# Kernel optimization log

Hardware: AMD Instinct MI355X
Metric: run time of the kernel (lower is better)

## Reference

```python
import jax, jax.numpy as jnp
import numpy as np

B = 8192          # number of nodes / batch
DEG = 32          # neighbors per node (fixed-degree instance of the ragged pattern)
E = B * DEG       # total neighbor rows
D = 256           # embedding_dim
A = 128           # attn_dim
ACT = 512         # action_dim
SLOPE = 0.2       # leakyrelu slope


def setup_inputs() -> dict:
    key = jax.random.key(0)
    ks = jax.random.split(key, 12)
    inp = {
        "state": jax.random.normal(ks[0], (B, 2 * D), jnp.float32),
        "now_embedding": jax.random.normal(ks[1], (B, D), jnp.float32),
        "neigh": jax.random.normal(ks[2], (E, D), jnp.float32),
        "seg_ids": jnp.repeat(jnp.arange(B, dtype=jnp.int32), DEG),  # sorted segment ids
        # attention projection Linear(D, A)
        "attn_w": jax.random.normal(ks[3], (D, A), jnp.float32) * (1.0 / np.sqrt(D)),
        "attn_b": jnp.zeros((A,), jnp.float32),
        # attn_weight Linear(2A, 1)
        "aw_w": jax.random.normal(ks[4], (2 * A, 1), jnp.float32) * (1.0 / np.sqrt(2 * A)),
        "aw_b": jnp.zeros((1,), jnp.float32),
        # MLP head
        "w1": jax.random.normal(ks[5], (3 * D, 512), jnp.float32) * (1.0 / np.sqrt(3 * D)),
        "b1": jnp.zeros((512,), jnp.float32),
        "w2": jax.random.normal(ks[6], (512, 1024), jnp.float32) * (1.0 / np.sqrt(512)),
        "b2": jnp.zeros((1024,), jnp.float32),
        "w3": jax.random.normal(ks[7], (1024, ACT), jnp.float32) * (1.0 / np.sqrt(1024)),
        "b3": jnp.zeros((ACT,), jnp.float32),
    }
    return inp


def reference(state, now_embedding, neigh, seg_ids, attn_w, attn_b, aw_w, aw_b,
              w1, b1, w2, b2, w3, b3):
    # project center and neighbor embeddings to attn space
    now_proj = now_embedding @ attn_w + attn_b          # [B, A]
    nb_proj = neigh @ attn_w + attn_b                   # [E, A]
    # attn_weight applied to concat([now_proj[seg], nb_proj]) == split matvec
    w_now, w_nb = aw_w[:A, 0], aw_w[A:, 0]              # [A], [A]
    scores = (now_proj @ w_now)[seg_ids] + nb_proj @ w_nb + aw_b[0]   # [E]
    scores = jnp.where(scores >= 0, scores, SLOPE * scores)           # LeakyReLU(0.2)
    # per-segment (per-node) softmax over neighbors
    seg_max = jax.ops.segment_max(scores, seg_ids, num_segments=B)
    e = jnp.exp(scores - seg_max[seg_ids])
    seg_sum = jax.ops.segment_sum(e, seg_ids, num_segments=B)
    alpha = e / seg_sum[seg_ids]                        # [E]
    # weighted aggregation of raw neighbor embeddings
    agg = jax.ops.segment_sum(alpha[:, None] * neigh, seg_ids, num_segments=B)  # [B, D]
    # MLP head (dropout prob = 0 -> identity)
    out = jnp.concatenate([state, agg], axis=1)         # [B, 3D]
    out = jax.nn.relu(out @ w1 + b1)
    out = jax.nn.relu(out @ w2 + b2)
    out = out @ w3 + b3
    return jax.nn.softmax(out, axis=-1)
```

## Files before the change

### kernel.cpp

```cpp
#include <hip/hip_runtime.h>
#include <hip/hip_bf16.h>

#define B_SEG  8192
#define DEG    32
#define D_DIM  256
#define TWO_D  512
#define H1     512
#define H2     1024
#define ACTD   512
#define SLOPE  0.2f

typedef __attribute__((ext_vector_type(8))) short bf16x8;
typedef __attribute__((ext_vector_type(4))) float f32x4;

#define OFF_VNOW  ((size_t)0)
#define OFF_VNB   ((size_t)1024)
#define OFF_CNST  ((size_t)2048)
#define OFF_W1T   ((size_t)4096)
#define OFF_W2T   (OFF_W1T + (size_t)768*512*2)
#define OFF_W3T   (OFF_W2T + (size_t)512*1024*2)
#define OFF_X1    (OFF_W3T + (size_t)1024*512*2)
#define OFF_X2    (OFF_X1 + (size_t)B_SEG*768*2)
#define OFF_X3    (OFF_X2 + (size_t)B_SEG*512*2)
#define OFF_LOG   (OFF_X3 + (size_t)B_SEG*1024*2)

typedef const unsigned int __attribute__((address_space(1)))* gas_ptr;
typedef unsigned int __attribute__((address_space(3)))* las_ptr;

__device__ __forceinline__ void gload_lds16(const void* g, void* l) {
    __builtin_amdgcn_global_load_lds((gas_ptr)g, (las_ptr)l, 16, 0, 0);
}

__global__ __launch_bounds__(256) void prep_all(
        const float* __restrict__ attn_w, const float* __restrict__ attn_b,
        const float* __restrict__ aw_w, const float* __restrict__ aw_b,
        const float* __restrict__ w1, const float* __restrict__ w2, const float* __restrict__ w3,
        float* __restrict__ vnow, float* __restrict__ vnb, float* __restrict__ cnst,
        __hip_bfloat16* __restrict__ w1T, __hip_bfloat16* __restrict__ w2T,
        __hip_bfloat16* __restrict__ w3T) {
    int bid = blockIdx.x;
    if (bid == 0) {
        const int d = threadIdx.x;
        float s0 = 0.f, s1 = 0.f;
        for (int a = 0; a < 128; ++a) {
            const float w = attn_w[d * 128 + a];
            s0 = fmaf(w, aw_w[a], s0);
            s1 = fmaf(w, aw_w[128 + a], s1);
        }
        vnow[d] = s0;
        vnb[d]  = s1;
        if (d == 0) {
            float c = aw_b[0];
            for (int a = 0; a < 128; ++a) c = fmaf(attn_b[a], aw_w[a] + aw_w[128 + a], c);
            cnst[0] = c;
        }
        return;
    }
    bid -= 1;
    const float* src;
    __hip_bfloat16* dst;
    int K, N;
    if (bid < 384)      { src = w1; dst = w1T; K = 768;  N = 512;  }
    else if (bid < 896) { bid -= 384; src = w2; dst = w2T; K = 512;  N = 1024; }
    else                { bid -= 896; src = w3; dst = w3T; K = 1024; N = 512;  }
    const int tk = K >> 5;
    const int bk = (bid % tk) * 32;
    const int bn = (bid / tk) * 32;

    __shared__ float tile[32][33];
    const int tx = threadIdx.x & 31;
    const int ty = threadIdx.x >> 5;
#pragma unroll
    for (int i = 0; i < 32; i += 8)
        tile[ty + i][tx] = src[(size_t)(bk + ty + i) * N + (bn + tx)];
    __syncthreads();
#pragma unroll
    for (int i = 0; i < 32; i += 8)
        dst[(size_t)(bn + ty + i) * K + (bk + tx)] = __float2bfloat16(tile[tx][ty + i]);
}

__global__ __launch_bounds__(256) void attn_fused(
        const float* __restrict__ state, const float* __restrict__ now_emb,
        const float* __restrict__ neigh, const float* __restrict__ vnow,
        const float* __restrict__ vnb, const float* __restrict__ cnst,
        __hip_bfloat16* __restrict__ X1) {
    const int b    = blockIdx.x;
    const int tid  = threadIdx.x;
    const int lane = tid & 63;
    const int w    = tid >> 6;
    const int l4   = lane * 4;

    __shared__ float s_score[DEG];
    __shared__ float s_now;
    __shared__ float s_part[4][D_DIM];

    const float4 vb = *(const float4*)&vnb[l4];
    float4 nv[8];
#pragma unroll
    for (int i = 0; i < 8; ++i) {
        const int e = w * 8 + i;
        nv[i] = *(const float4*)&neigh[((size_t)b * DEG + e) * D_DIM + l4];
        float p = nv[i].x * vb.x + nv[i].y * vb.y + nv[i].z * vb.z + nv[i].w * vb.w;
#pragma unroll
        for (int off = 32; off; off >>= 1) p += __shfl_xor(p, off);
        if (lane == 0) s_score[e] = p;
    }
    if (w == 0) {
        const float4 va = *(const float4*)&vnow[l4];
        const float4 ne = *(const float4*)&now_emb[(size_t)b * D_DIM + l4];
        float p = ne.x * va.x + ne.y * va.y + ne.z * va.z + ne.w * va.w;
#pragma unroll
        for (int off = 32; off; off >>= 1) p += __shfl_xor(p, off);
        if (lane == 0) s_now = p + cnst[0];
    }
    __syncthreads();

    if (w == 0) {
        float s = (lane < DEG) ? (s_score[lane] + s_now) : -3.4e38f;
        s = (s >= 0.f) ? s : SLOPE * s;
        float m = s;
#pragma unroll
        for (int off = 32; off; off >>= 1) m = fmaxf(m, __shfl_xor(m, off));
        const float e = (lane < DEG) ? expf(s - m) : 0.f;
        float t = e;
#pragma unroll
        for (int off = 32; off; off >>= 1) t += __shfl_xor(t, off);
        if (lane < DEG) s_score[lane] = e / t;
    }
    __syncthreads();

    float4 part = {0.f, 0.f, 0.f, 0.f};
#pragma unroll
    for (int i = 0; i < 8; ++i) {
        const float al = s_score[w * 8 + i];
        part.x = fmaf(al, nv[i].x, part.x);
        part.y = fmaf(al, nv[i].y, part.y);
        part.z = fmaf(al, nv[i].z, part.z);
        part.w = fmaf(al, nv[i].w, part.w);
    }
    *(float4*)&s_part[w][l4] = part;
    __syncthreads();

    const float a = s_part[0][tid] + s_part[1][tid] + s_part[2][tid] + s_part[3][tid];

    __hip_bfloat16* xrow = X1 + (size_t)b * 768;
    xrow[512 + tid] = __float2bfloat16(a);
    const float2 st = *(const float2*)&state[(size_t)b * TWO_D + 2 * tid];
    __hip_bfloat162 h;
    h.x = __float2bfloat16(st.x);
    h.y = __float2bfloat16(st.y);
    *(__hip_bfloat162*)&xrow[2 * tid] = h;
}

template <int RELU, int OUTF32>
__global__ __launch_bounds__(256) void gemm_mfma(
        const __hip_bfloat16* __restrict__ A, const __hip_bfloat16* __restrict__ BT,
        const float* __restrict__ bias, void* __restrict__ Cout, int N, int K) {
    __shared__ __hip_bfloat16 sA[64 * 32];
    __shared__ __hip_bfloat16 sB[128 * 32];

    const int tid  = threadIdx.x;
    const int lane = tid & 63;
    const int wv   = tid >> 6;
    const int wr   = wv >> 1;
    const int wc   = wv & 1;
    const size_t mBase = (size_t)blockIdx.x * 64;
    const size_t nBase = (size_t)blockIdx.y * 128;

    f32x4 acc[2][4];
#pragma unroll
    for (int r = 0; r < 2; ++r)
#pragma unroll
        for (int c = 0; c < 4; ++c) acc[r][c] = (f32x4){0.f, 0.f, 0.f, 0.f};

    const int srow = tid >> 2;
    const int sseg = tid & 3;
    const __hip_bfloat16* gA  = A  + (mBase + srow) * (size_t)K + sseg * 8;
    const __hip_bfloat16* gB0 = BT + (nBase + srow) * (size_t)K + sseg * 8;
    const __hip_bfloat16* gB1 = gB0 + (size_t)64 * K;
    char* ldsA = (char*)&sA[0] + tid * 16;
    char* ldsB = (char*)&sB[0] + tid * 16;

    const int fr  = lane & 15;
    const int fkb = (lane >> 4) * 16;

    for (int k0 = 0; k0 < K; k0 += 32) {
        gload_lds16(gA + k0, ldsA);
        gload_lds16(gB0 + k0, ldsB);
        gload_lds16(gB1 + k0, ldsB + 4096);
        __syncthreads();

        bf16x8 aF[2], bF[4];
#pragma unroll
        for (int r = 0; r < 2; ++r)
            aF[r] = *(const bf16x8*)((const char*)sA + (wr * 32 + r * 16 + fr) * 64 + fkb);
#pragma unroll
        for (int c = 0; c < 4; ++c)
            bF[c] = *(const bf16x8*)((const char*)sB + (wc * 64 + c * 16 + fr) * 64 + fkb);
#pragma unroll
        for (int r = 0; r < 2; ++r)
#pragma unroll
            for (int c = 0; c < 4; ++c)
                acc[r][c] = __builtin_amdgcn_mfma_f32_16x16x32_bf16(aF[r], bF[c], acc[r][c], 0, 0, 0);
        __syncthreads();
    }

    const int fq = lane >> 4;
#pragma unroll
    for (int r = 0; r < 2; ++r) {
#pragma unroll
        for (int c = 0; c < 4; ++c) {
            const size_t col = nBase + wc * 64 + c * 16 + fr;
            const float bcol = bias[col];
#pragma unroll
            for (int q = 0; q < 4; ++q) {
                const size_t row = mBase + wr * 32 + r * 16 + fq * 4 + q;
                float v = acc[r][c][q] + bcol;
                if (RELU) v = fmaxf(v, 0.f);
                if (OUTF32) ((float*)Cout)[row * N + col] = v;
                else ((__hip_bfloat16*)Cout)[row * N + col] = __float2bfloat16(v);
            }
        }
    }
}

__global__ __launch_bounds__(256) void softmax512(const float* __restrict__ logits,
                                                  float* __restrict__ out) {
    const int b    = blockIdx.x;
    const int tid  = threadIdx.x;
    const int lane = tid & 63;
    const int w    = tid >> 6;
    const float* row = logits + (size_t)b * ACTD;
    const float x0 = row[tid], x1 = row[tid + 256];
    float m = fmaxf(x0, x1);
#pragma unroll
    for (int off = 32; off; off >>= 1) m = fmaxf(m, __shfl_xor(m, off));
    __shared__ float sm[4], ss[4];
    if (lane == 0) sm[w] = m;
    __syncthreads();
    m = fmaxf(fmaxf(sm[0], sm[1]), fmaxf(sm[2], sm[3]));
    const float e0 = expf(x0 - m), e1 = expf(x1 - m);
    float t = e0 + e1;
#pragma unroll
    for (int off = 32; off; off >>= 1) t += __shfl_xor(t, off);
    if (lane == 0) ss[w] = t;
    __syncthreads();
    const float inv = 1.f / (ss[0] + ss[1] + ss[2] + ss[3]);
    out[(size_t)b * ACTD + tid]       = e0 * inv;
    out[(size_t)b * ACTD + tid + 256] = e1 * inv;
}

extern "C" void kernel_launch(void* const* d_in, const int* in_sizes, int n_in,
                              void* d_out, int out_size, void* d_ws, size_t ws_size,
                              hipStream_t stream) {
    const float* state   = (const float*)d_in[0];
    const float* now_emb = (const float*)d_in[1];
    const float* neigh   = (const float*)d_in[2];
    const float* attn_w  = (const float*)d_in[4];
    const float* attn_b  = (const float*)d_in[5];
    const float* aw_w    = (const float*)d_in[6];
    const float* aw_b    = (const float*)d_in[7];
    const float* w1      = (const float*)d_in[8];
    const float* b1      = (const float*)d_in[9];
    const float* w2      = (const float*)d_in[10];
    const float* b2      = (const float*)d_in[11];
    const float* w3      = (const float*)d_in[12];
    const float* b3      = (const float*)d_in[13];
    float* out = (float*)d_out;

    char* ws = (char*)d_ws;
    float*          vnow = (float*)(ws + OFF_VNOW);
    float*          vnb  = (float*)(ws + OFF_VNB);
    float*          cnst = (float*)(ws + OFF_CNST);
    __hip_bfloat16* w1T  = (__hip_bfloat16*)(ws + OFF_W1T);
    __hip_bfloat16* w2T  = (__hip_bfloat16*)(ws + OFF_W2T);
    __hip_bfloat16* w3T  = (__hip_bfloat16*)(ws + OFF_W3T);
    __hip_bfloat16* X1   = (__hip_bfloat16*)(ws + OFF_X1);
    __hip_bfloat16* X2   = (__hip_bfloat16*)(ws + OFF_X2);
    __hip_bfloat16* X3   = (__hip_bfloat16*)(ws + OFF_X3);
    float*          lgts = (float*)(ws + OFF_LOG);

    prep_all<<<1409, 256, 0, stream>>>(attn_w, attn_b, aw_w, aw_b, w1, w2, w3,
                                       vnow, vnb, cnst, w1T, w2T, w3T);
    attn_fused<<<B_SEG, 256, 0, stream>>>(state, now_emb, neigh, vnow, vnb, cnst, X1);
    gemm_mfma<1, 0><<<dim3(128, 4), 256, 0, stream>>>(X1, w1T, b1, (void*)X2, 512, 768);
    gemm_mfma<1, 0><<<dim3(128, 8), 256, 0, stream>>>(X2, w2T, b2, (void*)X3, 1024, 512);
    gemm_mfma<0, 1><<<dim3(128, 4), 256, 0, stream>>>(X3, w3T, b3, (void*)lgts, 512, 1024);
    softmax512<<<B_SEG, 256, 0, stream>>>(lgts, out);
}
```

Before: 141.7 us.

## Fuse final GEMM with row softmax and fold weight transposes into attention kernel

The last GEMM now has each 512-thread block compute a full 32x512 row slab and apply bias plus a row softmax in registers, using cross-wave reductions through LDS. This removes the fp32 logits round trip through global memory and the separate softmax launch. The weight transpose/bf16 cast blocks are appended to the attention kernel's grid so they run alongside attention work, leaving only a tiny one-block prep launch before it. In exchange, every GEMM3 block streams the whole w3T, so weight traffic rises, and with 256 blocks and no double buffering the fused GEMM may have less latency hiding.

```diff
diff --git a/kernel.cpp b/kernel.cpp
--- a/kernel.cpp
+++ b/kernel.cpp
@@ -5,8 +5,6 @@
 #define DEG    32
 #define D_DIM  256
 #define TWO_D  512
-#define H1     512
-#define H2     1024
 #define ACTD   512
 #define SLOPE  0.2f
 
@@ -22,7 +20,6 @@
 #define OFF_X1    (OFF_W3T + (size_t)1024*512*2)
 #define OFF_X2    (OFF_X1 + (size_t)B_SEG*768*2)
 #define OFF_X3    (OFF_X2 + (size_t)B_SEG*512*2)
-#define OFF_LOG   (OFF_X3 + (size_t)B_SEG*1024*2)
 
 typedef const unsigned int __attribute__((address_space(1)))* gas_ptr;
 typedef unsigned int __attribute__((address_space(3)))* las_ptr;
@@ -31,68 +28,71 @@
     __builtin_amdgcn_global_load_lds((gas_ptr)g, (las_ptr)l, 16, 0, 0);
 }
 
-__global__ __launch_bounds__(256) void prep_all(
+__global__ __launch_bounds__(256) void prep_vec(
         const float* __restrict__ attn_w, const float* __restrict__ attn_b,
         const float* __restrict__ aw_w, const float* __restrict__ aw_b,
-        const float* __restrict__ w1, const float* __restrict__ w2, const float* __restrict__ w3,
-        float* __restrict__ vnow, float* __restrict__ vnb, float* __restrict__ cnst,
-        __hip_bfloat16* __restrict__ w1T, __hip_bfloat16* __restrict__ w2T,
-        __hip_bfloat16* __restrict__ w3T) {
-    int bid = blockIdx.x;
-    if (bid == 0) {
-        const int d = threadIdx.x;
-        float s0 = 0.f, s1 = 0.f;
-        for (int a = 0; a < 128; ++a) {
-            const float w = attn_w[d * 128 + a];
-            s0 = fmaf(w, aw_w[a], s0);
-            s1 = fmaf(w, aw_w[128 + a], s1);
-        }
-        vnow[d] = s0;
-        vnb[d]  = s1;
-        if (d == 0) {
-            float c = aw_b[0];
-            for (int a = 0; a < 128; ++a) c = fmaf(attn_b[a], aw_w[a] + aw_w[128 + a], c);
-            cnst[0] = c;
-        }
-        return;
-    }
-    bid -= 1;
-    const float* src;
-    __hip_bfloat16* dst;
-    int K, N;
-    if (bid < 384)      { src = w1; dst = w1T; K = 768;  N = 512;  }
-    else if (bid < 896) { bid -= 384; src = w2; dst = w2T; K = 512;  N = 1024; }
-    else                { bid -= 896; src = w3; dst = w3T; K = 1024; N = 512;  }
-    const int tk = K >> 5;
-    const int bk = (bid % tk) * 32;
-    const int bn = (bid / tk) * 32;
-
-    __shared__ float tile[32][33];
-    const int tx = threadIdx.x & 31;
-    const int ty = threadIdx.x >> 5;
-#pragma unroll
-    for (int i = 0; i < 32; i += 8)
-        tile[ty + i][tx] = src[(size_t)(bk + ty + i) * N + (bn + tx)];
-    __syncthreads();
-#pragma unroll
-    for (int i = 0; i < 32; i += 8)
-        dst[(size_t)(bn + ty + i) * K + (bk + tx)] = __float2bfloat16(tile[tx][ty + i]);
-}
-
-__global__ __launch_bounds__(256) void attn_fused(
+        float* __restrict__ vnow, float* __restrict__ vnb, float* __restrict__ cnst) {
+    const int d = threadIdx.x;
+    float s0 = 0.f, s1 = 0.f;
+    for (int a = 0; a < 128; ++a) {
+        const float w = attn_w[d * 128 + a];
+        s0 = fmaf(w, aw_w[a], s0);
+        s1 = fmaf(w, aw_w[128 + a], s1);
+    }
+    vnow[d] = s0;
+    vnb[d]  = s1;
+    if (d == 0) {
+        float c = aw_b[0];
+        for (int a = 0; a < 128; ++a) c = fmaf(attn_b[a], aw_w[a] + aw_w[128 + a], c);
+        cnst[0] = c;
+    }
+}
+
+__global__ __launch_bounds__(256) void attn_tr(
         const float* __restrict__ state, const float* __restrict__ now_emb,
         const float* __restrict__ neigh, const float* __restrict__ vnow,
         const float* __restrict__ vnb, const float* __restrict__ cnst,
-        __hip_bfloat16* __restrict__ X1) {
-    const int b    = blockIdx.x;
+        __hip_bfloat16* __restrict__ X1,
+        const float* __restrict__ w1, const float* __restrict__ w2,
+        const float* __restrict__ w3,
+        __hip_bfloat16* __restrict__ w1T, __hip_bfloat16* __restrict__ w2T,
+        __hip_bfloat16* __restrict__ w3T) {
+    __shared__ __align__(16) float smem[1088];
+    const int bid = blockIdx.x;
+
+    if (bid >= B_SEG) {
+        int pb = bid - B_SEG;
+        const float* src;
+        __hip_bfloat16* dst;
+        int K, N;
+        if (pb < 384)      { src = w1; dst = w1T; K = 768;  N = 512;  }
+        else if (pb < 896) { pb -= 384; src = w2; dst = w2T; K = 512;  N = 1024; }
+        else               { pb -= 896; src = w3; dst = w3T; K = 1024; N = 512;  }
+        const int tk = K >> 5;
+        const int bk = (pb % tk) * 32;
+        const int bn = (pb / tk) * 32;
+        float (*tile)[33] = (float(*)[33])smem;
+        const int tx = threadIdx.x & 31;
+        const int ty = threadIdx.x >> 5;
+#pragma unroll
+        for (int i = 0; i < 32; i += 8)
+            tile[ty + i][tx] = src[(size_t)(bk + ty + i) * N + (bn + tx)];
+        __syncthreads();
+#pragma unroll
+        for (int i = 0; i < 32; i += 8)
+            dst[(size_t)(bn + ty + i) * K + (bk + tx)] = __float2bfloat16(tile[tx][ty + i]);
+        return;
+    }
+
+    const int b    = bid;
     const int tid  = threadIdx.x;
     const int lane = tid & 63;
     const int w    = tid >> 6;
     const int l4   = lane * 4;
 
-    __shared__ float s_score[DEG];
-    __shared__ float s_now;
-    __shared__ float s_part[4][D_DIM];
+    float* s_part  = smem;
+    float* s_score = smem + 1024;
+    float* s_now   = smem + 1056;
 
     const float4 vb = *(const float4*)&vnb[l4];
     float4 nv[8];
@@ -111,12 +111,12 @@
         float p = ne.x * va.x + ne.y * va.y + ne.z * va.z + ne.w * va.w;
 #pragma unroll
         for (int off = 32; off; off >>= 1) p += __shfl_xor(p, off);
-        if (lane == 0) s_now = p + cnst[0];
+        if (lane == 0) s_now[0] = p + cnst[0];
     }
     __syncthreads();
 
     if (w == 0) {
-        float s = (lane < DEG) ? (s_score[lane] + s_now) : -3.4e38f;
+        float s = (lane < DEG) ? (s_score[lane] + s_now[0]) : -3.4e38f;
         s = (s >= 0.f) ? s : SLOPE * s;
         float m = s;
 #pragma unroll
@@ -138,10 +138,11 @@
         part.z = fmaf(al, nv[i].z, part.z);
         part.w = fmaf(al, nv[i].w, part.w);
     }
-    *(float4*)&s_part[w][l4] = part;
-    __syncthreads();
-
-    const float a = s_part[0][tid] + s_part[1][tid] + s_part[2][tid] + s_part[3][tid];
+    *(float4*)&s_part[w * D_DIM + l4] = part;
+    __syncthreads();
+
+    const float a = s_part[tid] + s_part[D_DIM + tid] + s_part[2 * D_DIM + tid] +
+                    s_part[3 * D_DIM + tid];
 
     __hip_bfloat16* xrow = X1 + (size_t)b * 768;
     xrow[512 + tid] = __float2bfloat16(a);
@@ -224,30 +225,140 @@
     }
 }
 
-__global__ __launch_bounds__(256) void softmax512(const float* __restrict__ logits,
-                                                  float* __restrict__ out) {
-    const int b    = blockIdx.x;
+__global__ __launch_bounds__(512) void gemm3_softmax(
+        const __hip_bfloat16* __restrict__ A, const __hip_bfloat16* __restrict__ BT,
+        const float* __restrict__ bias, float* __restrict__ out) {
+    constexpr int K = 1024;
+    constexpr int N = 512;
+    __shared__ __hip_bfloat16 sA[32 * 32];
+    __shared__ __hip_bfloat16 sB[512 * 32];
+    __shared__ float s_max[8][32];
+    __shared__ float s_sum[8][32];
+    __shared__ float s_gmax[32];
+    __shared__ float s_ginv[32];
+
     const int tid  = threadIdx.x;
     const int lane = tid & 63;
-    const int w    = tid >> 6;
-    const float* row = logits + (size_t)b * ACTD;
-    const float x0 = row[tid], x1 = row[tid + 256];
-    float m = fmaxf(x0, x1);
-#pragma unroll
-    for (int off = 32; off; off >>= 1) m = fmaxf(m, __shfl_xor(m, off));
-    __shared__ float sm[4], ss[4];
-    if (lane == 0) sm[w] = m;
-    __syncthreads();
-    m = fmaxf(fmaxf(sm[0], sm[1]), fmaxf(sm[2], sm[3]));
-    const float e0 = expf(x0 - m), e1 = expf(x1 - m);
-    float t = e0 + e1;
-#pragma unroll
-    for (int off = 32; off; off >>= 1) t += __shfl_xor(t, off);
-    if (lane == 0) ss[w] = t;
-    __syncthreads();
-    const float inv = 1.f / (ss[0] + ss[1] + ss[2] + ss[3]);
-    out[(size_t)b * ACTD + tid]       = e0 * inv;
-    out[(size_t)b * ACTD + tid + 256] = e1 * inv;
+    const int wv   = tid >> 6;
+    const size_t mBase = (size_t)blockIdx.x * 32;
+
+    f32x4 acc[2][4];
+#pragma unroll
+    for (int r = 0; r < 2; ++r)
+#pragma unroll
+        for (int c = 0; c < 4; ++c) acc[r][c] = (f32x4){0.f, 0.f, 0.f, 0.f};
+
+    const __hip_bfloat16* gA = A + (mBase + (tid >> 2)) * (size_t)K + (tid & 3) * 8;
+    char* ldsA = (char*)&sA[0] + tid * 16;
+    const __hip_bfloat16* gB[4];
+    char* ldsB[4];
+#pragma unroll
+    for (int i = 0; i < 4; ++i) {
+        const int s = tid + i * 512;
+        gB[i]   = BT + (size_t)(s >> 2) * K + (s & 3) * 8;
+        ldsB[i] = (char*)&sB[0] + s * 16;
+    }
+
+    const int fr  = lane & 15;
+    const int fkb = (lane >> 4) * 16;
+
+    for (int k0 = 0; k0 < K; k0 += 32) {
+        if (tid < 128) gload_lds16(gA + k0, ldsA);
+#pragma unroll
+        for (int i = 0; i < 4; ++i) gload_lds16(gB[i] + k0, ldsB[i]);
+        __syncthreads();
+
+        bf16x8 aF[2], bF[4];
+#pragma unroll
+        for (int r = 0; r < 2; ++r)
+            aF[r] = *(const bf16x8*)((const char*)sA + (r * 16 + fr) * 64 + fkb);
+#pragma unroll
+        for (int c = 0; c < 4; ++c)
+            bF[c] = *(const bf16x8*)((const char*)sB + (wv * 64 + c * 16 + fr) * 64 + fkb);
+#pragma unroll
+        for (int r = 0; r < 2; ++r)
+#pragma unroll
+            for (int c = 0; c < 4; ++c)
+                acc[r][c] = __builtin_amdgcn_mfma_f32_16x16x32_bf16(aF[r], bF[c], acc[r][c], 0, 0, 0);
+        __syncthreads();
+    }
+
+    const int fq = lane >> 4;
+    float bcol[4];
+#pragma unroll
+    for (int c = 0; c < 4; ++c) bcol[c] = bias[wv * 64 + c * 16 + fr];
+
+    float rm[2][4];
+#pragma unroll
+    for (int r = 0; r < 2; ++r)
+#pragma unroll
+        for (int q = 0; q < 4; ++q) {
+            float m = -3.4e38f;
+#pragma unroll
+            for (int c = 0; c < 4; ++c) {
+                acc[r][c][q] += bcol[c];
+                m = fmaxf(m, acc[r][c][q]);
+            }
+#pragma unroll
+            for (int off = 8; off; off >>= 1) m = fmaxf(m, __shfl_xor(m, off));
+            rm[r][q] = m;
+        }
+    if (fr == 0) {
+#pragma unroll
+        for (int r = 0; r < 2; ++r)
+#pragma unroll
+            for (int q = 0; q < 4; ++q) s_max[wv][r * 16 + fq * 4 + q] = rm[r][q];
+    }
+    __syncthreads();
+    if (tid < 32) {
+        float m = s_max[0][tid];
+#pragma unroll
+        for (int w2_ = 1; w2_ < 8; ++w2_) m = fmaxf(m, s_max[w2_][tid]);
+        s_gmax[tid] = m;
+    }
+    __syncthreads();
+
+    float rs[2][4];
+#pragma unroll
+    for (int r = 0; r < 2; ++r)
+#pragma unroll
+        for (int q = 0; q < 4; ++q) {
+            const float gm = s_gmax[r * 16 + fq * 4 + q];
+            float s = 0.f;
+#pragma unroll
+            for (int c = 0; c < 4; ++c) {
+                acc[r][c][q] = expf(acc[r][c][q] - gm);
+                s += acc[r][c][q];
+            }
+#pragma unroll
+            for (int off = 8; off; off >>= 1) s += __shfl_xor(s, off);
+            rs[r][q] = s;
+        }
+    if (fr == 0) {
+#pragma unroll
+        for (int r = 0; r < 2; ++r)
+#pragma unroll
+            for (int q = 0; q < 4; ++q) s_sum[wv][r * 16 + fq * 4 + q] = rs[r][q];
+    }
+    __syncthreads();
+    if (tid < 32) {
+        float t = s_sum[0][tid];
+#pragma unroll
+        for (int w2_ = 1; w2_ < 8; ++w2_) t += s_sum[w2_][tid];
+        s_ginv[tid] = 1.f / t;
+    }
+    __syncthreads();
+
+#pragma unroll
+    for (int r = 0; r < 2; ++r)
+#pragma unroll
+        for (int q = 0; q < 4; ++q) {
+            const float inv = s_ginv[r * 16 + fq * 4 + q];
+            const size_t row = mBase + r * 16 + fq * 4 + q;
+#pragma unroll
+            for (int c = 0; c < 4; ++c)
+                out[row * N + wv * 64 + c * 16 + fr] = acc[r][c][q] * inv;
+        }
 }
 
 extern "C" void kernel_launch(void* const* d_in, const int* in_sizes, int n_in,
@@ -278,13 +389,11 @@
     __hip_bfloat16* X1   = (__hip_bfloat16*)(ws + OFF_X1);
     __hip_bfloat16* X2   = (__hip_bfloat16*)(ws + OFF_X2);
     __hip_bfloat16* X3   = (__hip_bfloat16*)(ws + OFF_X3);
-    float*          lgts = (float*)(ws + OFF_LOG);
-
-    prep_all<<<1409, 256, 0, stream>>>(attn_w, attn_b, aw_w, aw_b, w1, w2, w3,
-                                       vnow, vnb, cnst, w1T, w2T, w3T);
-    attn_fused<<<B_SEG, 256, 0, stream>>>(state, now_emb, neigh, vnow, vnb, cnst, X1);
+
+    prep_vec<<<1, 256, 0, stream>>>(attn_w, attn_b, aw_w, aw_b, vnow, vnb, cnst);
+    attn_tr<<<B_SEG + 1408, 256, 0, stream>>>(state, now_emb, neigh, vnow, vnb, cnst, X1,
+                                              w1, w2, w3, w1T, w2T, w3T);
     gemm_mfma<1, 0><<<dim3(128, 4), 256, 0, stream>>>(X1, w1T, b1, (void*)X2, 512, 768);
     gemm_mfma<1, 0><<<dim3(128, 8), 256, 0, stream>>>(X2, w2T, b2, (void*)X3, 1024, 512);
-    gemm_mfma<0, 1><<<dim3(128, 4), 256, 0, stream>>>(X3, w3T, b3, (void*)lgts, 512, 1024);
-    softmax512<<<B_SEG, 256, 0, stream>>>(lgts, out);
-}
+    gemm3_softmax<<<256, 512, 0, stream>>>(X3, w3T, b3, out);
+}
```

Result: slower. 149.5 us (+5.5%).

## Double-buffer GEMM LDS tiles with BK=64 and XOR-swizzled layout

Applied to the files above, without the earlier changes.

Rewrites the MFMA GEMM so it double-buffers the LDS tiles. The next K-tile's global-to-LDS loads are issued before computing on the current one, and the K step grows from 32 to 64. The LDS layout is XOR-swizzled by row to avoid bank conflicts on the fragment reads. The goal is to overlap memory latency with MFMA work and to halve the barrier count, in exchange for more LDS per block (48KB), which may lower occupancy.

```diff
diff --git a/kernel.cpp b/kernel.cpp
--- a/kernel.cpp
+++ b/kernel.cpp
@@ -5,8 +5,6 @@
 #define DEG    32
 #define D_DIM  256
 #define TWO_D  512
-#define H1     512
-#define H2     1024
 #define ACTD   512
 #define SLOPE  0.2f
 
@@ -153,11 +151,11 @@
 }
 
 template <int RELU, int OUTF32>
-__global__ __launch_bounds__(256) void gemm_mfma(
+__global__ __launch_bounds__(256) void gemm_db(
         const __hip_bfloat16* __restrict__ A, const __hip_bfloat16* __restrict__ BT,
         const float* __restrict__ bias, void* __restrict__ Cout, int N, int K) {
-    __shared__ __hip_bfloat16 sA[64 * 32];
-    __shared__ __hip_bfloat16 sB[128 * 32];
+    __shared__ __hip_bfloat16 sA[2][64 * 64];
+    __shared__ __hip_bfloat16 sB[2][128 * 64];
 
     const int tid  = threadIdx.x;
     const int lane = tid & 63;
@@ -166,6 +164,7 @@
     const int wc   = wv & 1;
     const size_t mBase = (size_t)blockIdx.x * 64;
     const size_t nBase = (size_t)blockIdx.y * 128;
+    const size_t Kb = (size_t)K * 2;
 
     f32x4 acc[2][4];
 #pragma unroll
@@ -173,37 +172,65 @@
 #pragma unroll
         for (int c = 0; c < 4; ++c) acc[r][c] = (f32x4){0.f, 0.f, 0.f, 0.f};
 
-    const int srow = tid >> 2;
-    const int sseg = tid & 3;
-    const __hip_bfloat16* gA  = A  + (mBase + srow) * (size_t)K + sseg * 8;
-    const __hip_bfloat16* gB0 = BT + (nBase + srow) * (size_t)K + sseg * 8;
-    const __hip_bfloat16* gB1 = gB0 + (size_t)64 * K;
-    char* ldsA = (char*)&sA[0] + tid * 16;
-    char* ldsB = (char*)&sB[0] + tid * 16;
+    const int srow  = tid >> 3;
+    const int kbLog = ((tid & 7) ^ (srow & 7)) << 4;
+    const char* gA = (const char*)A  + (mBase + srow) * Kb + kbLog;
+    const char* gB = (const char*)BT + (nBase + srow) * Kb + kbLog;
+    char* lA = (char*)&sA[0][0] + tid * 16;
+    char* lB = (char*)&sB[0][0] + tid * 16;
 
     const int fr  = lane & 15;
     const int fkb = (lane >> 4) * 16;
-
-    for (int k0 = 0; k0 < K; k0 += 32) {
-        gload_lds16(gA + k0, ldsA);
-        gload_lds16(gB0 + k0, ldsB);
-        gload_lds16(gB1 + k0, ldsB + 4096);
+    const char* sAb = (const char*)&sA[0][0];
+    const char* sBb = (const char*)&sB[0][0];
+
+    const int nk = K >> 6;
+
+#define STAGE(T, BUF) do {                                                         \
+        const size_t kOff = (size_t)(T) * 128;                                     \
+        gload_lds16(gA + kOff,           lA + (BUF) * 8192);                       \
+        gload_lds16(gA + kOff + 32 * Kb, lA + (BUF) * 8192 + 4096);                \
+        gload_lds16(gB + kOff,           lB + (BUF) * 16384);                      \
+        gload_lds16(gB + kOff + 32 * Kb, lB + (BUF) * 16384 + 4096);               \
+        gload_lds16(gB + kOff + 64 * Kb, lB + (BUF) * 16384 + 8192);               \
+        gload_lds16(gB + kOff + 96 * Kb, lB + (BUF) * 16384 + 12288);              \
+    } while (0)
+
+#define SWZ(ROW, KB) ((ROW) * 128 + ((KB) ^ (((ROW) & 7) << 4)))
+
+    STAGE(0, 0);
+    __syncthreads();
+
+    int cur = 0;
+    for (int t = 0; t < nk; ++t) {
+        if (t + 1 < nk) STAGE(t + 1, cur ^ 1);
+
+        const char* bufA = sAb + cur * 8192;
+        const char* bufB = sBb + cur * 16384;
+#pragma unroll
+        for (int ks = 0; ks < 2; ++ks) {
+            bf16x8 aF[2], bF[4];
+#pragma unroll
+            for (int r = 0; r < 2; ++r) {
+                const int row = wr * 32 + r * 16 + fr;
+                aF[r] = *(const bf16x8*)(bufA + SWZ(row, ks * 64 + fkb));
+            }
+#pragma unroll
+            for (int c = 0; c < 4; ++c) {
+                const int row = wc * 64 + c * 16 + fr;
+                bF[c] = *(const bf16x8*)(bufB + SWZ(row, ks * 64 + fkb));
+            }
+#pragma unroll
+            for (int r = 0; r < 2; ++r)
+#pragma unroll
+                for (int c = 0; c < 4; ++c)
+                    acc[r][c] = __builtin_amdgcn_mfma_f32_16x16x32_bf16(aF[r], bF[c], acc[r][c], 0, 0, 0);
+        }
         __syncthreads();
-
-        bf16x8 aF[2], bF[4];
-#pragma unroll
-        for (int r = 0; r < 2; ++r)
-            aF[r] = *(const bf16x8*)((const char*)sA + (wr * 32 + r * 16 + fr) * 64 + fkb);
-#pragma unroll
-        for (int c = 0; c < 4; ++c)
-            bF[c] = *(const bf16x8*)((const char*)sB + (wc * 64 + c * 16 + fr) * 64 + fkb);
-#pragma unroll
-        for (int r = 0; r < 2; ++r)
-#pragma unroll
-            for (int c = 0; c < 4; ++c)
-                acc[r][c] = __builtin_amdgcn_mfma_f32_16x16x32_bf16(aF[r], bF[c], acc[r][c], 0, 0, 0);
-        __syncthreads();
-    }
+        cur ^= 1;
+    }
+#undef STAGE
+#undef SWZ
 
     const int fq = lane >> 4;
 #pragma unroll
@@ -283,8 +310,8 @@
     prep_all<<<1409, 256, 0, stream>>>(attn_w, attn_b, aw_w, aw_b, w1, w2, w3,
                                        vnow, vnb, cnst, w1T, w2T, w3T);
     attn_fused<<<B_SEG, 256, 0, stream>>>(state, now_emb, neigh, vnow, vnb, cnst, X1);
-    gemm_mfma<1, 0><<<dim3(128, 4), 256, 0, stream>>>(X1, w1T, b1, (void*)X2, 512, 768);
-    gemm_mfma<1, 0><<<dim3(128, 8), 256, 0, stream>>>(X2, w2T, b2, (void*)X3, 1024, 512);
-    gemm_mfma<0, 1><<<dim3(128, 4), 256, 0, stream>>>(X3, w3T, b3, (void*)lgts, 512, 1024);
+    gemm_db<1, 0><<<dim3(128, 4), 256, 0, stream>>>(X1, w1T, b1, (void*)X2, 512, 768);
+    gemm_db<1, 0><<<dim3(128, 8), 256, 0, stream>>>(X2, w2T, b2, (void*)X3, 1024, 512);
+    gemm_db<0, 1><<<dim3(128, 4), 256, 0, stream>>>(X3, w3T, b3, (void*)lgts, 512, 1024);
     softmax512<<<B_SEG, 256, 0, stream>>>(lgts, out);
 }
```

New measurement: 134.6 us. 1.05x faster.
